# Performance work log

Hardware: AMD Instinct MI355X
Metric: run time of the kernel (lower is better)

## Reference

```python
import jax, jax.numpy as jnp
import numpy as np

B, T, D, P, C = 65536, 3, 512, 32, 10  # batch, views, x_dim, p_dim, num_classes

def setup_inputs() -> dict:
    key = jax.random.key(0)
    ks = jax.random.split(key, 6)
    return {
        "x": jax.random.normal(ks[0], (B, T, D), dtype=jnp.float32),
        "Wk": jax.random.normal(ks[1], (P, D), dtype=jnp.float32) * (1.0 / np.sqrt(D)),
        "Wv": jax.random.normal(ks[2], (P, D), dtype=jnp.float32) * (1.0 / np.sqrt(D)),
        "Wq": jax.random.normal(ks[3], (P, T * D), dtype=jnp.float32) * (1.0 / np.sqrt(T * D)),
        "Wfc": jax.random.normal(ks[4], (C, P), dtype=jnp.float32) * (1.0 / np.sqrt(P)),
        "bfc": jax.random.normal(ks[5], (C,), dtype=jnp.float32) * 0.01,
    }

def reference(x, Wk, Wv, Wq, Wfc, bfc):
    # x: [B, 3, D]. Per-sample: k_i = Wk x_i, v_i = Wv x_i, q = Wq concat(x1,x2,x3)
    k = jnp.einsum('btd,pd->btp', x, Wk)                 # [B,3,P]
    v = jnp.einsum('btd,pd->btp', x, Wv)                 # [B,3,P]
    q = jnp.einsum('bf,pf->bp', x.reshape(x.shape[0], -1), Wq)  # [B,P]
    a = jax.nn.softmax(jnp.einsum('bp,btp->bt', q, k), axis=-1)  # 3-way softmax [B,3]
    c = jnp.einsum('bt,btp->bp', a, v)                   # weighted sum [B,P]
    return c @ Wfc.T + bfc                               # [B,C]
```

## Files before the change

### kernel.cpp

```cpp
#include <hip/hip_runtime.h>


typedef __attribute__((ext_vector_type(4))) float  f32x4;
typedef __attribute__((ext_vector_type(8))) _Float16 h16x8;

#define T_VIEWS 3
#define D_DIM   512
#define P_DIM   32
#define C_DIM   10
#define NROWS   80
#define NT      5
#define KC      16
#define WAVES_PER_BLOCK 4
#define SAMPLES_PER_BLOCK (16 * WAVES_PER_BLOCK)

__global__ void build_weights(const float* __restrict__ Wk,
                              const float* __restrict__ Wv,
                              const float* __restrict__ Wq,
                              const float* __restrict__ Wfc,
                              _Float16* __restrict__ Wf) {
    const int row = blockIdx.x;
    const int t   = row / NROWS;
    const int j   = row % NROWS;
    const int d   = threadIdx.x;
    float val;
    if (j < 32) {
        val = Wk[j * D_DIM + d];
    } else if (j < 64) {
        const int p = j - 32;
        val = Wq[p * (T_VIEWS * D_DIM) + t * D_DIM + d];
    } else if (j < 64 + C_DIM) {
        const int i = j - 64;
        float s = 0.f;
        #pragma unroll
        for (int p = 0; p < P_DIM; ++p)
            s += Wfc[i * P_DIM + p] * Wv[p * D_DIM + d];
        val = s;
    } else {
        val = 0.f;
    }
    const int n = j >> 4, coln = j & 15;
    const int kc = d >> 5, r = d & 31;
    const int quad = (r >> 2) & 3;
    const int jj   = ((r >> 4) << 2) | (r & 3);
    const size_t addr = (size_t)((((t * KC + kc) * NT + n) * 64) + quad * 16 + coln) * 8 + jj;
    Wf[addr] = (_Float16)val;
}

__global__ __launch_bounds__(256, 4) void attn_fused(
        const float* __restrict__ x,
        const _Float16* __restrict__ Wf,
        const float* __restrict__ bfc,
        float* __restrict__ out) {
    const int lane = threadIdx.x & 63;
    const int wave = threadIdx.x >> 6;
    const int col  = lane & 15;
    const int quad = lane >> 4;
    const int row_base = blockIdx.x * SAMPLES_PER_BLOCK + wave * 16;

    f32x4 acc_k[3][2];
    f32x4 acc_q[2];
    f32x4 acc_y[3];
    #pragma unroll
    for (int t = 0; t < 3; ++t) {
        acc_k[t][0] = (f32x4)0.f;
        acc_k[t][1] = (f32x4)0.f;
        acc_y[t]    = (f32x4)0.f;
    }
    acc_q[0] = (f32x4)0.f;
    acc_q[1] = (f32x4)0.f;

    const float* xbase = x + (size_t)(row_base + col) * (T_VIEWS * D_DIM) + quad * 4;
    const _Float16* wt = Wf + lane * 8;

    #pragma unroll
    for (int t = 0; t < 3; ++t) {
        #pragma unroll 2
        for (int kc = 0; kc < KC; ++kc) {
            h16x8 b[NT];
            #pragma unroll
            for (int n = 0; n < NT; ++n)
                b[n] = *(const h16x8*)(wt + (size_t)(((t * KC + kc) * NT + n)) * 512);
            const float* xp = xbase + t * D_DIM + kc * 32;
            const f32x4 x0 = __builtin_nontemporal_load((const f32x4*)xp);
            const f32x4 x1 = __builtin_nontemporal_load((const f32x4*)(xp + 16));
            h16x8 a;
            #pragma unroll
            for (int i = 0; i < 4; ++i) {
                a[i]     = (_Float16)x0[i];
                a[i + 4] = (_Float16)x1[i];
            }
            acc_k[t][0] = __builtin_amdgcn_mfma_f32_16x16x32_f16(a, b[0], acc_k[t][0], 0, 0, 0);
            acc_k[t][1] = __builtin_amdgcn_mfma_f32_16x16x32_f16(a, b[1], acc_k[t][1], 0, 0, 0);
            acc_q[0]    = __builtin_amdgcn_mfma_f32_16x16x32_f16(a, b[2], acc_q[0],    0, 0, 0);
            acc_q[1]    = __builtin_amdgcn_mfma_f32_16x16x32_f16(a, b[3], acc_q[1],    0, 0, 0);
            acc_y[t]    = __builtin_amdgcn_mfma_f32_16x16x32_f16(a, b[4], acc_y[t],    0, 0, 0);
        }
    }

    const float bias = (col < C_DIM) ? bfc[col] : 0.f;

    float outv[4];
    #pragma unroll
    for (int r = 0; r < 4; ++r) {
        const float qa = acc_q[0][r];
        const float qb = acc_q[1][r];
        float s0 = qa * acc_k[0][0][r] + qb * acc_k[0][1][r];
        float s1 = qa * acc_k[1][0][r] + qb * acc_k[1][1][r];
        float s2 = qa * acc_k[2][0][r] + qb * acc_k[2][1][r];
        #pragma unroll
        for (int msk = 1; msk <= 8; msk <<= 1) {
            s0 += __shfl_xor(s0, msk, 64);
            s1 += __shfl_xor(s1, msk, 64);
            s2 += __shfl_xor(s2, msk, 64);
        }
        const float mx = fmaxf(s0, fmaxf(s1, s2));
        const float e0 = __expf(s0 - mx);
        const float e1 = __expf(s1 - mx);
        const float e2 = __expf(s2 - mx);
        const float inv = 1.f / (e0 + e1 + e2);
        outv[r] = (e0 * acc_y[0][r] + e1 * acc_y[1][r] + e2 * acc_y[2][r]) * inv + bias;
    }
    if (col < C_DIM) {
        const int b0 = row_base + quad * 4;
        #pragma unroll
        for (int r = 0; r < 4; ++r)
            out[(size_t)(b0 + r) * C_DIM + col] = outv[r];
    }
}

extern "C" void kernel_launch(void* const* d_in, const int* in_sizes, int n_in,
                              void* d_out, int out_size, void* d_ws, size_t ws_size,
                              hipStream_t stream) {
    const float* x   = (const float*)d_in[0];
    const float* Wk  = (const float*)d_in[1];
    const float* Wv  = (const float*)d_in[2];
    const float* Wq  = (const float*)d_in[3];
    const float* Wfc = (const float*)d_in[4];
    const float* bfc = (const float*)d_in[5];
    _Float16* Wf = (_Float16*)d_ws;

    hipLaunchKernelGGL(build_weights, dim3(T_VIEWS * NROWS), dim3(D_DIM), 0, stream,
                       Wk, Wv, Wq, Wfc, Wf);

    const int B_TOTAL = in_sizes[0] / (T_VIEWS * D_DIM);
    const int blocks = B_TOTAL / SAMPLES_PER_BLOCK;
    hipLaunchKernelGGL(attn_fused, dim3(blocks), dim3(256), 0, stream,
                       x, Wf, bfc, (float*)d_out);
}
```

Baseline: 561.5 us.

## Stage fused weights through double-buffered LDS via async global_load_lds

Each block now loads the packed fp16 weight tiles into a double-buffered shared-memory ring with global_load_lds, prefetching the next chunk of four k-steps while the current chunk feeds the MFMAs. The waves then read B operands from LDS instead of each wave fetching them from global/L2. This cuts redundant L2 weight traffic across the four waves and overlaps the weight fetch with compute. In exchange it adds a block-wide barrier per chunk and 40 KB of LDS per block, which may limit occupancy below the launch-bounds target of 4 blocks per CU.

```diff
diff --git a/kernel.cpp b/kernel.cpp
--- a/kernel.cpp
+++ b/kernel.cpp
@@ -11,6 +11,11 @@
 #define NROWS   80
 #define NT      5
 #define KC      16
+#define NSTEPS  48
+#define JPER    4
+#define NSUPER  (NSTEPS/JPER)
+#define STEP_B  (NT*1024)
+#define CHUNK_B (JPER*STEP_B)
 #define WAVES_PER_BLOCK 4
 #define SAMPLES_PER_BLOCK (16 * WAVES_PER_BLOCK)
 
@@ -52,6 +57,8 @@
         const _Float16* __restrict__ Wf,
         const float* __restrict__ bfc,
         float* __restrict__ out) {
+    __shared__ char lds[2 * CHUNK_B];
+
     const int lane = threadIdx.x & 63;
     const int wave = threadIdx.x >> 6;
     const int col  = lane & 15;
@@ -71,19 +78,44 @@
     acc_q[1] = (f32x4)0.f;
 
     const float* xbase = x + (size_t)(row_base + col) * (T_VIEWS * D_DIM) + quad * 4;
-    const _Float16* wt = Wf + lane * 8;
+    const char*  wf   = (const char*)Wf + lane * 16;
 
     #pragma unroll
-    for (int t = 0; t < 3; ++t) {
-        #pragma unroll 2
-        for (int kc = 0; kc < KC; ++kc) {
+    for (int i = 0; i < 5; ++i) {
+        const int idx = wave * 5 + i;
+        __builtin_amdgcn_global_load_lds(
+            (const __attribute__((address_space(1))) void*)(wf + (size_t)idx * 1024),
+            (__attribute__((address_space(3))) void*)(lds + idx * 1024),
+            16, 0, 0);
+    }
+    __syncthreads();
+
+    for (int u = 0; u < NSUPER; ++u) {
+        const int cbuf = u & 1;
+        const int nbuf = cbuf ^ 1;
+        if (u + 1 < NSUPER) {
+            #pragma unroll
+            for (int i = 0; i < 5; ++i) {
+                const int idx = wave * 5 + i;
+                const size_t gb = (size_t)(u + 1) * CHUNK_B + (size_t)idx * 1024;
+                __builtin_amdgcn_global_load_lds(
+                    (const __attribute__((address_space(1))) void*)(wf + gb),
+                    (__attribute__((address_space(3))) void*)(lds + nbuf * CHUNK_B + idx * 1024),
+                    16, 0, 0);
+            }
+        }
+        #pragma unroll
+        for (int j = 0; j < JPER; ++j) {
+            const int s  = u * JPER + j;
+            const int t  = s >> 4;
+            const int kc = s & 15;
+            const float* xp = xbase + t * D_DIM + kc * 32;
+            const f32x4 x0 = __builtin_nontemporal_load((const f32x4*)xp);
+            const f32x4 x1 = __builtin_nontemporal_load((const f32x4*)(xp + 16));
             h16x8 b[NT];
             #pragma unroll
             for (int n = 0; n < NT; ++n)
-                b[n] = *(const h16x8*)(wt + (size_t)(((t * KC + kc) * NT + n)) * 512);
-            const float* xp = xbase + t * D_DIM + kc * 32;
-            const f32x4 x0 = __builtin_nontemporal_load((const f32x4*)xp);
-            const f32x4 x1 = __builtin_nontemporal_load((const f32x4*)(xp + 16));
+                b[n] = *(const h16x8*)(lds + cbuf * CHUNK_B + j * STEP_B + n * 1024 + lane * 16);
             h16x8 a;
             #pragma unroll
             for (int i = 0; i < 4; ++i) {
@@ -96,6 +128,7 @@
             acc_q[1]    = __builtin_amdgcn_mfma_f32_16x16x32_f16(a, b[3], acc_q[1],    0, 0, 0);
             acc_y[t]    = __builtin_amdgcn_mfma_f32_16x16x32_f16(a, b[4], acc_y[t],    0, 0, 0);
         }
+        __syncthreads();
     }
 
     const float bias = (col < C_DIM) ? bfc[col] : 0.f;
```

Result: faster. 533.2 us (-5.0%).

## Stage x windows into LDS with double-buffered global_load_lds per single-wave block

Applied to the files above, without the earlier changes.

Each block is now one wave handling 16 samples. The x rows are streamed in 256-float windows straight into LDS through global_load_lds, double-buffered so the next window loads while the current one feeds the MFMAs. An XOR swizzle on the LDS layout avoids bank conflicts. The aim is coalesced full-row loads that overlap with compute, replacing the strided per-lane direct global loads. The cost is 32KB of LDS per block, which may limit occupancy, plus a sync per window.

```diff
diff --git a/kernel.cpp b/kernel.cpp
--- a/kernel.cpp
+++ b/kernel.cpp
@@ -6,13 +6,17 @@
 
 #define T_VIEWS 3
 #define D_DIM   512
+#define ROW_F   (T_VIEWS * D_DIM)
 #define P_DIM   32
 #define C_DIM   10
 #define NROWS   80
 #define NT      5
 #define KC      16
-#define WAVES_PER_BLOCK 4
-#define SAMPLES_PER_BLOCK (16 * WAVES_PER_BLOCK)
+#define M_SAMP  16
+#define NWIN    6
+#define WIN_F   256
+#define JW      8
+#define WIN_BYTES (M_SAMP * 1024)
 
 __global__ void build_weights(const float* __restrict__ Wk,
                               const float* __restrict__ Wv,
@@ -47,16 +51,17 @@
     Wf[addr] = (_Float16)val;
 }
 
-__global__ __launch_bounds__(256, 4) void attn_fused(
+__global__ __launch_bounds__(64, 2) void attn_fused(
         const float* __restrict__ x,
         const _Float16* __restrict__ Wf,
         const float* __restrict__ bfc,
         float* __restrict__ out) {
-    const int lane = threadIdx.x & 63;
-    const int wave = threadIdx.x >> 6;
+    __shared__ char lds[2 * WIN_BYTES];
+
+    const int lane = threadIdx.x;
     const int col  = lane & 15;
     const int quad = lane >> 4;
-    const int row_base = blockIdx.x * SAMPLES_PER_BLOCK + wave * 16;
+    const int row_base = blockIdx.x * M_SAMP;
 
     f32x4 acc_k[3][2];
     f32x4 acc_q[2];
@@ -70,20 +75,37 @@
     acc_q[0] = (f32x4)0.f;
     acc_q[1] = (f32x4)0.f;
 
-    const float* xbase = x + (size_t)(row_base + col) * (T_VIEWS * D_DIM) + quad * 4;
-    const _Float16* wt = Wf + lane * 8;
+    auto STAGE = [&](int w, char* buf) {
+        #pragma unroll
+        for (int i = 0; i < M_SAMP; ++i) {
+            const float* src = x + (size_t)(row_base + i) * ROW_F + w * WIN_F
+                                 + ((lane ^ (i & 7)) << 2);
+            __builtin_amdgcn_global_load_lds(
+                (const __attribute__((address_space(1))) void*)src,
+                (__attribute__((address_space(3))) void*)(buf + i * 1024),
+                16, 0, 0);
+        }
+    };
+
+    STAGE(0, lds);
 
     #pragma unroll
-    for (int t = 0; t < 3; ++t) {
-        #pragma unroll 2
-        for (int kc = 0; kc < KC; ++kc) {
+    for (int w = 0; w < NWIN; ++w) {
+        __syncthreads();
+        if (w + 1 < NWIN)
+            STAGE(w + 1, lds + ((w + 1) & 1) * WIN_BYTES);
+        const char* buf = lds + (w & 1) * WIN_BYTES;
+        const int t = w >> 1;
+        const _Float16* wbase = Wf + (size_t)(w * JW) * NT * 512 + lane * 8;
+
+        #pragma unroll
+        for (int j = 0; j < JW; ++j) {
             h16x8 b[NT];
             #pragma unroll
             for (int n = 0; n < NT; ++n)
-                b[n] = *(const h16x8*)(wt + (size_t)(((t * KC + kc) * NT + n)) * 512);
-            const float* xp = xbase + t * D_DIM + kc * 32;
-            const f32x4 x0 = __builtin_nontemporal_load((const f32x4*)xp);
-            const f32x4 x1 = __builtin_nontemporal_load((const f32x4*)(xp + 16));
+                b[n] = *(const h16x8*)(wbase + (size_t)(j * NT + n) * 512);
+            const f32x4 x0 = *(const f32x4*)(buf + col * 1024 + (((j * 8 + quad)     ^ (col & 7)) << 4));
+            const f32x4 x1 = *(const f32x4*)(buf + col * 1024 + (((j * 8 + 4 + quad) ^ (col & 7)) << 4));
             h16x8 a;
             #pragma unroll
             for (int i = 0; i < 4; ++i) {
@@ -144,7 +166,7 @@
                        Wk, Wv, Wq, Wfc, Wf);
 
     const int B_TOTAL = in_sizes[0] / (T_VIEWS * D_DIM);
-    const int blocks = B_TOTAL / SAMPLES_PER_BLOCK;
-    hipLaunchKernelGGL(attn_fused, dim3(blocks), dim3(256), 0, stream,
+    const int blocks = B_TOTAL / M_SAMP;
+    hipLaunchKernelGGL(attn_fused, dim3(blocks), dim3(64), 0, stream,
                        x, Wf, bfc, (float*)d_out);
 }
```

New measurement: 543.4 us. 3.2% less time.
